# Performance work log

Hardware: AMD Instinct MI355X
Metric: run time of the kernel (lower is better)

## Reference

```python
import jax, jax.numpy as jnp
import numpy as np

B, N, DIM = 4, 1024, 768
HEADS, DIM_HEAD = 12, 64
INNER = HEADS * DIM_HEAD  # 768
SCALE = DIM ** -0.5


def setup_inputs() -> dict:
    key = jax.random.key(0)
    ks = jax.random.split(key, 5)
    return {
        "x": jax.random.normal(ks[0], (B, N, DIM), dtype=jnp.float32),
        "pos_embedding": jax.random.normal(ks[1], (B, N, DIM), dtype=jnp.float32),
        "w_qkv": jax.random.normal(ks[2], (DIM, 3 * INNER), dtype=jnp.float32) * (DIM ** -0.5),
        "w_qk_pos": jax.random.normal(ks[3], (DIM, 2 * INNER), dtype=jnp.float32) * (DIM ** -0.5),
        "w_out": jax.random.normal(ks[4], (INNER, DIM), dtype=jnp.float32) * (INNER ** -0.5),
        "b_out": jnp.zeros((DIM,), dtype=jnp.float32),
    }


def _split_heads(t):
    # [b, n, h*d] -> [b, h, n, d]
    b, n, _ = t.shape
    return t.reshape(b, n, HEADS, DIM_HEAD).transpose(0, 2, 1, 3)


def reference(x, pos_embedding, w_qkv, w_qk_pos, w_out, b_out):
    qkv = x @ w_qkv  # [b, n, 3*inner]
    q, k, v = (_split_heads(t) for t in jnp.split(qkv, 3, axis=-1))
    qk_pos = pos_embedding @ w_qk_pos  # [b, n, 2*inner]
    q_pos, k_pos = (_split_heads(t) for t in jnp.split(qk_pos, 2, axis=-1))

    dots = jnp.einsum('bhid,bhjd->bhij', q, k) * SCALE
    dots_pos = jnp.einsum('bhid,bhjd->bhij', q_pos, k_pos) * SCALE
    dots = (dots + dots_pos) * 0.5  # averaged content+positional scores

    attn = jax.nn.softmax(dots, axis=-1)
    out = jnp.einsum('bhij,bhjd->bhid', attn, v)
    out = out.transpose(0, 2, 1, 3).reshape(x.shape[0], x.shape[1], INNER)
    return out @ w_out + b_out
```

## Files before the change

kernel.cpp:

```cpp
#include <hip/hip_runtime.h>
#include <cstdint>
#include <cstddef>

typedef __bf16 bf16;
typedef __bf16 bf16x8 __attribute__((ext_vector_type(8)));
typedef __bf16 bf16x4v __attribute__((ext_vector_type(4)));
typedef float  f32x4  __attribute__((ext_vector_type(4)));

#define MFMA(a, b, c) __builtin_amdgcn_mfma_f32_16x16x32_bf16((a), (b), (c), 0, 0, 0)

typedef __attribute__((address_space(3))) unsigned int  lds_u32;
typedef __attribute__((address_space(1))) unsigned int glob_u32;


__global__ void k_cvt2(const float* __restrict__ x, const float* __restrict__ pos,
                       bf16* __restrict__ xb, bf16* __restrict__ posb) {
    int i = blockIdx.x * 256 + threadIdx.x;
    const float* in = x; bf16* out = xb;
    if (i >= 786432) { i -= 786432; in = pos; out = posb; }
    float4 v = reinterpret_cast<const float4*>(in)[i];
    bf16x4v o; o[0] = (bf16)v.x; o[1] = (bf16)v.y; o[2] = (bf16)v.z; o[3] = (bf16)v.w;
    reinterpret_cast<bf16x4v*>(out)[i] = o;
}

__global__ void k_tr(const float* __restrict__ w_qkv, const float* __restrict__ w_qk_pos,
                     const float* __restrict__ w_out,
                     bf16* __restrict__ wqkvT, bf16* __restrict__ wqkposT,
                     bf16* __restrict__ woutT) {
    __shared__ float t[32][33];
    int bx = blockIdx.x;
    const float* in; bf16* out; int N;
    if (bx < 72)       { in = w_qkv;    out = wqkvT;   N = 2304; }
    else if (bx < 120) { in = w_qk_pos; out = wqkposT; N = 1536; bx -= 72; }
    else               { in = w_out;    out = woutT;   N = 768;  bx -= 120; }
    const int n0 = bx * 32, k0 = blockIdx.y * 32;
    const int tx = threadIdx.x & 31, ty = threadIdx.x >> 5;
#pragma unroll
    for (int r = 0; r < 32; r += 8)
        t[ty + r][tx] = in[(size_t)(k0 + ty + r) * N + n0 + tx];
    __syncthreads();
#pragma unroll
    for (int r = 0; r < 32; r += 8)
        out[(size_t)(n0 + ty + r) * 768 + k0 + tx] = (bf16)t[tx][ty + r];
}

__launch_bounds__(256, 3)
__global__ void k_gemm12(const bf16* __restrict__ xb, const bf16* __restrict__ posb,
                         const bf16* __restrict__ wqkvT, const bf16* __restrict__ wqkposT,
                         bf16* __restrict__ qcat, bf16* __restrict__ kcat,
                         bf16* __restrict__ vT) {
    __shared__ bf16 lA[2][128][32];
    __shared__ bf16 lB[2][128][32];

    const int tid  = threadIdx.x;
    const int lane = tid & 63, wave = tid >> 6;
    const int quad = lane >> 4, col = lane & 15;
    const int sw2  = (col >> 1) & 3;
    const int wm = (wave >> 1) * 64, wn = (wave & 1) * 64;

    const int fid = blockIdx.x;
    const int xcd = fid & 7, s = fid >> 3;
    const int sx = s % 15, sy = s / 15;
    int bx = (xcd & 1) * 15 + sx;
    const int by = (xcd >> 1) * 8 + sy;

    int mode, nBase;
    const bf16 *A, *BT;
    if (bx < 18) { mode = 0; A = xb;   BT = wqkvT;   nBase = bx * 128; }
    else         { mode = 1; A = posb; BT = wqkposT; nBase = (bx - 18) * 128; }
    const int mBase = by * 128;

    const bf16* Ap = A  + (size_t)mBase * 768;
    const bf16* Bp = BT + (size_t)nBase * 768;

#define STAGE12(buf, k0)                                                        \
    _Pragma("unroll")                                                           \
    for (int j = 0; j < 2; ++j) {                                               \
        int idx = (wave * 2 + j) * 64 + lane;                                   \
        int row = idx >> 2, c = (idx & 3) ^ ((row >> 1) & 3);                   \
        __builtin_amdgcn_global_load_lds(                                       \
            (const glob_u32*)(Ap + (size_t)row * 768 + (k0) + c * 8),           \
            (lds_u32*)((char*)&lA[buf][0][0] + (wave * 2 + j) * 1024), 16, 0, 0);\
        __builtin_amdgcn_global_load_lds(                                       \
            (const glob_u32*)(Bp + (size_t)row * 768 + (k0) + c * 8),           \
            (lds_u32*)((char*)&lB[buf][0][0] + (wave * 2 + j) * 1024), 16, 0, 0);\
    }

    f32x4 acc[4][4];
#pragma unroll
    for (int mi = 0; mi < 4; ++mi)
#pragma unroll
        for (int ni = 0; ni < 4; ++ni) acc[mi][ni] = f32x4{0.f, 0.f, 0.f, 0.f};

    STAGE12(0, 0)
    for (int it = 0; it < 24; ++it) {
        const int cur = it & 1, nxt = cur ^ 1;
        __syncthreads();
        if (it < 23) STAGE12(nxt, (it + 1) * 32)

        bf16x8 af[4], bfg[4];
#pragma unroll
        for (int mi = 0; mi < 4; ++mi)
            af[mi]  = *(const bf16x8*)&lA[cur][wm + mi * 16 + col][(quad ^ sw2) * 8];
#pragma unroll
        for (int ni = 0; ni < 4; ++ni)
            bfg[ni] = *(const bf16x8*)&lB[cur][wn + ni * 16 + col][(quad ^ sw2) * 8];
#pragma unroll
        for (int mi = 0; mi < 4; ++mi)
#pragma unroll
            for (int ni = 0; ni < 4; ++ni)
                acc[mi][ni] = MFMA(af[mi], bfg[ni], acc[mi][ni]);
    }
#undef STAGE12

    const int bb = mBase >> 10;
    const int sr0 = (mBase & 1023) + wm + quad * 4;
#pragma unroll
    for (int ni = 0; ni < 4; ++ni) {
        const int nb = nBase + wn + ni * 16;
        const int which = (mode == 0) ? (nb >= 1536 ? 2 : (nb >= 768 ? 1 : 0))
                                      : (nb >= 768 ? 1 : 0);
        const int rem = nb - which * 768;
        const int hh = rem >> 6, dd0 = rem & 63;
        const size_t hb = (size_t)(bb * 12 + hh);
        if (mode == 0 && which == 2) {
            bf16* dstv = vT + (hb * 64 + dd0 + col) * 1024 + sr0;
#pragma unroll
            for (int mi = 0; mi < 4; ++mi) {
                bf16x4v pk;
#pragma unroll
                for (int r = 0; r < 4; ++r) pk[r] = (bf16)acc[mi][ni][r];
                *(bf16x4v*)(dstv + mi * 16) = pk;
            }
        } else {
            bf16* dstq = (which == 0 ? qcat : kcat)
                       + (hb * 1024 + sr0) * 128 + (mode == 1 ? 64 : 0) + dd0 + col;
#pragma unroll
            for (int mi = 0; mi < 4; ++mi)
#pragma unroll
                for (int r = 0; r < 4; ++r)
                    dstq[(size_t)(mi * 16 + r) * 128] = (bf16)acc[mi][ni][r];
        }
    }
}

__launch_bounds__(256, 3)
__global__ void k_attn(const bf16* __restrict__ qcat, const bf16* __restrict__ kcat,
                       const bf16* __restrict__ vT, bf16* __restrict__ attn_out) {
    __shared__ bf16 lK[2][64][128];
    __shared__ bf16 lV[2][64][64];
    __shared__ bf16 lP[4][16][40];

    const int tid  = threadIdx.x;
    const int lane = tid & 63, wave = tid >> 6;
    const int quad = lane >> 4, col = lane & 15;
    const int sw   = col & 7;

    const int fid = blockIdx.x;
    const int xcd = fid & 7, s = fid >> 3;
    const int qt = s & 15;
    const int unit = (s >> 4) * 8 + xcd;
    const int b = unit / 12, h = unit % 12;

    const size_t hrow = (size_t)(b * 12 + h) * 1024;
    const bf16* Kb = kcat + hrow * 128;
    const bf16* Vb = vT + (size_t)(b * 12 + h) * 64 * 1024;

    const int kidx = wave * 256 + lane;
    const int vidx = wave * 128 + lane;

#define STAGE_K(buf, kv0)                                                      \
    _Pragma("unroll")                                                          \
    for (int j = 0; j < 4; ++j) {                                              \
        int idx = kidx + j * 64;                                               \
        int row = idx >> 4, c = idx & 15, csrc = c ^ (row & 7);                \
        __builtin_amdgcn_global_load_lds(                                      \
            (const glob_u32*)(Kb + (size_t)((kv0) + row) * 128 + csrc * 8),    \
            (lds_u32*)(&lK[buf][0][0] + (wave * 4 + j) * 512), 16, 0, 0);      \
    }
#define STAGE_V(buf, kv0)                                                      \
    _Pragma("unroll")                                                          \
    for (int j = 0; j < 2; ++j) {                                              \
        int idx = vidx + j * 64;                                               \
        int row = idx >> 3, c = idx & 7, csrc = c ^ (row & 7);                 \
        __builtin_amdgcn_global_load_lds(                                      \
            (const glob_u32*)(Vb + (size_t)row * 1024 + (kv0) + csrc * 8),     \
            (lds_u32*)(&lV[buf][0][0] + (wave * 2 + j) * 512), 16, 0, 0);      \
    }

    bf16x8 qf[4];
    {
        const bf16* qrow = qcat + (hrow + qt * 64 + wave * 16 + col) * 128;
#pragma unroll
        for (int f = 0; f < 4; ++f) qf[f] = *(const bf16x8*)(qrow + f * 32 + quad * 8);
    }

    f32x4 o[4];
#pragma unroll
    for (int t = 0; t < 4; ++t) o[t] = f32x4{0.f, 0.f, 0.f, 0.f};
    float lsum[4] = {0.f, 0.f, 0.f, 0.f};
    const float c2 = 0.018042195912f * 1.44269504089f;

    STAGE_K(0, 0)
    STAGE_V(0, 0)

    for (int it = 0; it < 16; ++it) {
        const int cur = it & 1, nxt = cur ^ 1;
        __syncthreads();
        if (it < 15) {
            const int kv1 = (it + 1) * 64;
            STAGE_K(nxt, kv1)
            STAGE_V(nxt, kv1)
        }

        f32x4 s4[4];
#pragma unroll
        for (int t = 0; t < 4; ++t) s4[t] = f32x4{0.f, 0.f, 0.f, 0.f};
#pragma unroll
        for (int t = 0; t < 4; ++t)
#pragma unroll
            for (int f = 0; f < 4; ++f) {
                bf16x8 kf = *(const bf16x8*)&lK[cur][t * 16 + col][((f * 4 + quad) ^ sw) * 8];
                s4[t] = MFMA(qf[f], kf, s4[t]);
            }

#pragma unroll
        for (int t = 0; t < 4; ++t)
#pragma unroll
            for (int r = 0; r < 4; ++r) s4[t][r] = exp2f(s4[t][r] * c2);
#pragma unroll
        for (int r = 0; r < 4; ++r)
            lsum[r] += (s4[0][r] + s4[1][r]) + (s4[2][r] + s4[3][r]);

#pragma unroll
        for (int half = 0; half < 2; ++half) {
#pragma unroll
            for (int r = 0; r < 4; ++r)
#pragma unroll
                for (int t2 = 0; t2 < 2; ++t2)
                    lP[wave][quad * 4 + r][t2 * 16 + col] = (bf16)s4[half * 2 + t2][r];
            bf16x8 pf = *(const bf16x8*)&lP[wave][col][quad * 8];
#pragma unroll
            for (int t = 0; t < 4; ++t) {
                bf16x8 vf = *(const bf16x8*)&lV[cur][t * 16 + col][((half * 4 + quad) ^ sw) * 8];
                o[t] = MFMA(pf, vf, o[t]);
            }
        }
    }

#pragma unroll
    for (int r = 0; r < 4; ++r) {
        float l = lsum[r];
#pragma unroll
        for (int off = 1; off < 16; off <<= 1) l += __shfl_xor(l, off, 64);
        float inv = 1.f / l;
        int row = qt * 64 + wave * 16 + quad * 4 + r;
#pragma unroll
        for (int t = 0; t < 4; ++t)
            attn_out[((size_t)b * 1024 + row) * 768 + h * 64 + t * 16 + col] =
                (bf16)(o[t][r] * inv);
    }
#undef STAGE_K
#undef STAGE_V
}

__launch_bounds__(256, 3)
__global__ void k_gemm_out(const bf16* __restrict__ aout, const bf16* __restrict__ woutT,
                           const float* __restrict__ bias, float* __restrict__ out) {
    __shared__ bf16 lA[2][128][32];
    __shared__ bf16 lB[2][64][32];

    const int tid  = threadIdx.x;
    const int lane = tid & 63, wave = tid >> 6;
    const int quad = lane >> 4, col = lane & 15;
    const int sw2  = (col >> 1) & 3;
    const int wm = (wave >> 1) * 64, wn = (wave & 1) * 32;

    const int fid = blockIdx.x;
    const int xcd = fid & 7, s = fid >> 3;
    const int sx = s % 6, sy = s / 6;
    const int bx = (xcd & 1) * 6 + sx;
    const int by = (xcd >> 1) * 8 + sy;

    const int mBase = by * 128, nBase = bx * 64;

    const bf16* Ap = aout  + (size_t)mBase * 768;
    const bf16* Bp = woutT + (size_t)nBase * 768;

#define STAGE_O(buf, k0)                                                        \
    _Pragma("unroll")                                                           \
    for (int j = 0; j < 2; ++j) {                                               \
        int idx = (wave * 2 + j) * 64 + lane;                                   \
        int row = idx >> 2, c = (idx & 3) ^ ((row >> 1) & 3);                   \
        __builtin_amdgcn_global_load_lds(                                       \
            (const glob_u32*)(Ap + (size_t)row * 768 + (k0) + c * 8),           \
            (lds_u32*)((char*)&lA[buf][0][0] + (wave * 2 + j) * 1024), 16, 0, 0);\
    }                                                                           \
    {                                                                           \
        int idx = wave * 64 + lane;                                             \
        int row = idx >> 2, c = (idx & 3) ^ ((row >> 1) & 3);                   \
        __builtin_amdgcn_global_load_lds(                                       \
            (const glob_u32*)(Bp + (size_t)row * 768 + (k0) + c * 8),           \
            (lds_u32*)((char*)&lB[buf][0][0] + wave * 1024), 16, 0, 0);         \
    }

    f32x4 acc[4][2];
#pragma unroll
    for (int mi = 0; mi < 4; ++mi)
#pragma unroll
        for (int ni = 0; ni < 2; ++ni) acc[mi][ni] = f32x4{0.f, 0.f, 0.f, 0.f};

    STAGE_O(0, 0)
    for (int it = 0; it < 24; ++it) {
        const int cur = it & 1, nxt = cur ^ 1;
        __syncthreads();
        if (it < 23) STAGE_O(nxt, (it + 1) * 32)

        bf16x8 af[4], bfg[2];
#pragma unroll
        for (int mi = 0; mi < 4; ++mi)
            af[mi]  = *(const bf16x8*)&lA[cur][wm + mi * 16 + col][(quad ^ sw2) * 8];
#pragma unroll
        for (int ni = 0; ni < 2; ++ni)
            bfg[ni] = *(const bf16x8*)&lB[cur][wn + ni * 16 + col][(quad ^ sw2) * 8];
#pragma unroll
        for (int mi = 0; mi < 4; ++mi)
#pragma unroll
            for (int ni = 0; ni < 2; ++ni)
                acc[mi][ni] = MFMA(af[mi], bfg[ni], acc[mi][ni]);
    }
#undef STAGE_O

#pragma unroll
    for (int mi = 0; mi < 4; ++mi)
#pragma unroll
        for (int ni = 0; ni < 2; ++ni)
#pragma unroll
            for (int r = 0; r < 4; ++r) {
                int m = mBase + wm + mi * 16 + quad * 4 + r;
                int n = nBase + wn + ni * 16 + col;
                out[(size_t)m * 768 + n] = acc[mi][ni][r] + bias[n];
            }
}

extern "C" void kernel_launch(void* const* d_in, const int* in_sizes, int n_in,
                              void* d_out, int out_size, void* d_ws, size_t ws_size,
                              hipStream_t stream) {
    const float* x        = (const float*)d_in[0];
    const float* pos      = (const float*)d_in[1];
    const float* w_qkv    = (const float*)d_in[2];
    const float* w_qk_pos = (const float*)d_in[3];
    const float* w_out    = (const float*)d_in[4];
    const float* b_out    = (const float*)d_in[5];
    float* out = (float*)d_out;

    char* ws = (char*)d_ws;
    bf16* xb      = (bf16*)(ws);
    bf16* posb    = (bf16*)(ws + 6291456);
    bf16* wqkvT   = (bf16*)(ws + 12582912);
    bf16* wqkposT = (bf16*)(ws + 16121856);
    bf16* woutT   = (bf16*)(ws + 18481152);
    bf16* qcat    = (bf16*)(ws + 19660800);
    bf16* kcat    = (bf16*)(ws + 32243712);
    bf16* vT      = (bf16*)(ws + 44826624);
    bf16* aout    = (bf16*)(ws + 51118080);

    k_cvt2<<<6144, 256, 0, stream>>>(x, pos, xb, posb);
    k_tr<<<dim3(144, 24), 256, 0, stream>>>(w_qkv, w_qk_pos, w_out, wqkvT, wqkposT, woutT);
    k_gemm12<<<960, 256, 0, stream>>>(xb, posb, wqkvT, wqkposT, qcat, kcat, vT);
    k_attn<<<768, 256, 0, stream>>>(qcat, kcat, vT, aout);
    k_gemm_out<<<384, 256, 0, stream>>>(aout, woutT, b_out, out);
}
```

Measured before the change: 191.6 us.

## Split attention KV range across waves with register operands and LDS reduction

The attention kernel now has each wave own a slice of the key/value sequence for all 64 queries, instead of each wave owning 16 query rows and sweeping every key. K and V fragments are read straight from global memory into registers, so LDS staging and per-iteration barriers are gone. The softmax probabilities stay in registers as MFMA operands by computing S transposed (K·Q), which removes the LDS round-trip for P. Partial outputs and row sums are combined across waves through a float LDS reduction at the end. The softmax scale is folded into Q at the projection GEMM, and occupancy is lowered to 2 blocks per SM because of larger register and LDS use; uncoalesced global K/V loads add risk.

```diff
diff --git a/kernel.cpp b/kernel.cpp
--- a/kernel.cpp
+++ b/kernel.cpp
@@ -113,6 +113,7 @@
     }
 #undef STAGE12
 
+    const float c2s = 0.018042195912f * 1.44269504089f;
     const int bb = mBase >> 10;
     const int sr0 = (mBase & 1023) + wm + quad * 4;
 #pragma unroll
@@ -133,28 +134,28 @@
                 *(bf16x4v*)(dstv + mi * 16) = pk;
             }
         } else {
+            const float scl = (which == 0) ? c2s : 1.0f;
             bf16* dstq = (which == 0 ? qcat : kcat)
                        + (hb * 1024 + sr0) * 128 + (mode == 1 ? 64 : 0) + dd0 + col;
 #pragma unroll
             for (int mi = 0; mi < 4; ++mi)
 #pragma unroll
                 for (int r = 0; r < 4; ++r)
-                    dstq[(size_t)(mi * 16 + r) * 128] = (bf16)acc[mi][ni][r];
-        }
-    }
-}
-
-__launch_bounds__(256, 3)
+                    dstq[(size_t)(mi * 16 + r) * 128] = (bf16)(acc[mi][ni][r] * scl);
+        }
+    }
+}
+
+__launch_bounds__(256, 2)
 __global__ void k_attn(const bf16* __restrict__ qcat, const bf16* __restrict__ kcat,
                        const bf16* __restrict__ vT, bf16* __restrict__ attn_out) {
-    __shared__ bf16 lK[2][64][128];
-    __shared__ bf16 lV[2][64][64];
-    __shared__ bf16 lP[4][16][40];
+    __shared__ float lRed[4][64][68];
+    __shared__ float lS[16][64];
+    __shared__ float lSinv[64];
 
     const int tid  = threadIdx.x;
     const int lane = tid & 63, wave = tid >> 6;
     const int quad = lane >> 4, col = lane & 15;
-    const int sw   = col & 7;
 
     const int fid = blockIdx.x;
     const int xcd = fid & 7, s = fid >> 3;
@@ -162,106 +163,109 @@
     const int unit = (s >> 4) * 8 + xcd;
     const int b = unit / 12, h = unit % 12;
 
-    const size_t hrow = (size_t)(b * 12 + h) * 1024;
-    const bf16* Kb = kcat + hrow * 128;
-    const bf16* Vb = vT + (size_t)(b * 12 + h) * 64 * 1024;
-
-    const int kidx = wave * 256 + lane;
-    const int vidx = wave * 128 + lane;
-
-#define STAGE_K(buf, kv0)                                                      \
-    _Pragma("unroll")                                                          \
-    for (int j = 0; j < 4; ++j) {                                              \
-        int idx = kidx + j * 64;                                               \
-        int row = idx >> 4, c = idx & 15, csrc = c ^ (row & 7);                \
-        __builtin_amdgcn_global_load_lds(                                      \
-            (const glob_u32*)(Kb + (size_t)((kv0) + row) * 128 + csrc * 8),    \
-            (lds_u32*)(&lK[buf][0][0] + (wave * 4 + j) * 512), 16, 0, 0);      \
-    }
-#define STAGE_V(buf, kv0)                                                      \
-    _Pragma("unroll")                                                          \
-    for (int j = 0; j < 2; ++j) {                                              \
-        int idx = vidx + j * 64;                                               \
-        int row = idx >> 3, c = idx & 7, csrc = c ^ (row & 7);                 \
-        __builtin_amdgcn_global_load_lds(                                      \
-            (const glob_u32*)(Vb + (size_t)row * 1024 + (kv0) + csrc * 8),     \
-            (lds_u32*)(&lV[buf][0][0] + (wave * 2 + j) * 512), 16, 0, 0);      \
-    }
-
-    bf16x8 qf[4];
-    {
-        const bf16* qrow = qcat + (hrow + qt * 64 + wave * 16 + col) * 128;
-#pragma unroll
-        for (int f = 0; f < 4; ++f) qf[f] = *(const bf16x8*)(qrow + f * 32 + quad * 8);
-    }
-
-    f32x4 o[4];
-#pragma unroll
-    for (int t = 0; t < 4; ++t) o[t] = f32x4{0.f, 0.f, 0.f, 0.f};
-    float lsum[4] = {0.f, 0.f, 0.f, 0.f};
-    const float c2 = 0.018042195912f * 1.44269504089f;
-
-    STAGE_K(0, 0)
-    STAGE_V(0, 0)
-
-    for (int it = 0; it < 16; ++it) {
-        const int cur = it & 1, nxt = cur ^ 1;
-        __syncthreads();
-        if (it < 15) {
-            const int kv1 = (it + 1) * 64;
-            STAGE_K(nxt, kv1)
-            STAGE_V(nxt, kv1)
-        }
-
-        f32x4 s4[4];
-#pragma unroll
-        for (int t = 0; t < 4; ++t) s4[t] = f32x4{0.f, 0.f, 0.f, 0.f};
-#pragma unroll
-        for (int t = 0; t < 4; ++t)
-#pragma unroll
-            for (int f = 0; f < 4; ++f) {
-                bf16x8 kf = *(const bf16x8*)&lK[cur][t * 16 + col][((f * 4 + quad) ^ sw) * 8];
-                s4[t] = MFMA(qf[f], kf, s4[t]);
-            }
-
-#pragma unroll
-        for (int t = 0; t < 4; ++t)
-#pragma unroll
-            for (int r = 0; r < 4; ++r) s4[t][r] = exp2f(s4[t][r] * c2);
-#pragma unroll
-        for (int r = 0; r < 4; ++r)
-            lsum[r] += (s4[0][r] + s4[1][r]) + (s4[2][r] + s4[3][r]);
-
-#pragma unroll
-        for (int half = 0; half < 2; ++half) {
-#pragma unroll
-            for (int r = 0; r < 4; ++r)
-#pragma unroll
-                for (int t2 = 0; t2 < 2; ++t2)
-                    lP[wave][quad * 4 + r][t2 * 16 + col] = (bf16)s4[half * 2 + t2][r];
-            bf16x8 pf = *(const bf16x8*)&lP[wave][col][quad * 8];
-#pragma unroll
-            for (int t = 0; t < 4; ++t) {
-                bf16x8 vf = *(const bf16x8*)&lV[cur][t * 16 + col][((half * 4 + quad) ^ sw) * 8];
-                o[t] = MFMA(pf, vf, o[t]);
-            }
-        }
-    }
-
-#pragma unroll
-    for (int r = 0; r < 4; ++r) {
-        float l = lsum[r];
-#pragma unroll
-        for (int off = 1; off < 16; off <<= 1) l += __shfl_xor(l, off, 64);
-        float inv = 1.f / l;
-        int row = qt * 64 + wave * 16 + quad * 4 + r;
-#pragma unroll
-        for (int t = 0; t < 4; ++t)
-            attn_out[((size_t)b * 1024 + row) * 768 + h * 64 + t * 16 + col] =
-                (bf16)(o[t][r] * inv);
-    }
-#undef STAGE_K
-#undef STAGE_V
+    const bf16* Qb = qcat + (size_t)unit * 1024 * 128;
+    const bf16* Kb = kcat + (size_t)unit * 1024 * 128;
+    const bf16* Vb = vT   + (size_t)unit * 64 * 1024;
+
+    bf16x8 qb[4][4];
+#pragma unroll
+    for (int nt = 0; nt < 4; ++nt) {
+        const bf16* qrow = Qb + (size_t)(qt * 64 + nt * 16 + col) * 128;
+#pragma unroll
+        for (int f = 0; f < 4; ++f)
+            qb[nt][f] = *(const bf16x8*)(qrow + f * 32 + quad * 8);
+    }
+
+    f32x4 o[4][4];
+#pragma unroll
+    for (int vt = 0; vt < 4; ++vt)
+#pragma unroll
+        for (int nt = 0; nt < 4; ++nt) o[vt][nt] = f32x4{0.f, 0.f, 0.f, 0.f};
+    float ps[4] = {0.f, 0.f, 0.f, 0.f};
+
+    const int kvw = wave * 16;
+
+    for (int itp = 0; itp < 8; ++itp) {
+        const int kvA = itp * 128 + kvw;
+        const int kvB = kvA + 64;
+
+        bf16x8 kfA[4], kfB[4];
+#pragma unroll
+        for (int f = 0; f < 4; ++f) {
+            kfA[f] = *(const bf16x8*)(Kb + (size_t)(kvA + col) * 128 + f * 32 + quad * 8);
+            kfB[f] = *(const bf16x8*)(Kb + (size_t)(kvB + col) * 128 + f * 32 + quad * 8);
+        }
+        bf16x8 vf[4];
+#pragma unroll
+        for (int vt = 0; vt < 4; ++vt) {
+            bf16x4v va = *(const bf16x4v*)(Vb + (size_t)(vt * 16 + col) * 1024 + kvA + quad * 4);
+            bf16x4v vb = *(const bf16x4v*)(Vb + (size_t)(vt * 16 + col) * 1024 + kvB + quad * 4);
+#pragma unroll
+            for (int i = 0; i < 4; ++i) { vf[vt][i] = va[i]; vf[vt][4 + i] = vb[i]; }
+        }
+
+        bf16x8 pbf[4];
+#pragma unroll
+        for (int nt = 0; nt < 4; ++nt) {
+            f32x4 st = f32x4{0.f, 0.f, 0.f, 0.f};
+#pragma unroll
+            for (int f = 0; f < 4; ++f) st = MFMA(kfA[f], qb[nt][f], st);
+            float p0 = exp2f(st[0]), p1 = exp2f(st[1]);
+            float p2 = exp2f(st[2]), p3 = exp2f(st[3]);
+            ps[nt] += (p0 + p1) + (p2 + p3);
+            pbf[nt][0] = (bf16)p0; pbf[nt][1] = (bf16)p1;
+            pbf[nt][2] = (bf16)p2; pbf[nt][3] = (bf16)p3;
+        }
+#pragma unroll
+        for (int nt = 0; nt < 4; ++nt) {
+            f32x4 st = f32x4{0.f, 0.f, 0.f, 0.f};
+#pragma unroll
+            for (int f = 0; f < 4; ++f) st = MFMA(kfB[f], qb[nt][f], st);
+            float p0 = exp2f(st[0]), p1 = exp2f(st[1]);
+            float p2 = exp2f(st[2]), p3 = exp2f(st[3]);
+            ps[nt] += (p0 + p1) + (p2 + p3);
+            pbf[nt][4] = (bf16)p0; pbf[nt][5] = (bf16)p1;
+            pbf[nt][6] = (bf16)p2; pbf[nt][7] = (bf16)p3;
+        }
+#pragma unroll
+        for (int vt = 0; vt < 4; ++vt)
+#pragma unroll
+            for (int nt = 0; nt < 4; ++nt)
+                o[vt][nt] = MFMA(vf[vt], pbf[nt], o[vt][nt]);
+    }
+
+#pragma unroll
+    for (int vt = 0; vt < 4; ++vt)
+#pragma unroll
+        for (int nt = 0; nt < 4; ++nt)
+            *(f32x4*)&lRed[wave][nt * 16 + col][vt * 16 + quad * 4] = o[vt][nt];
+#pragma unroll
+    for (int nt = 0; nt < 4; ++nt)
+        lS[wave * 4 + quad][nt * 16 + col] = ps[nt];
+    __syncthreads();
+
+    if (tid < 64) {
+        float t = 0.f;
+#pragma unroll
+        for (int w = 0; w < 16; ++w) t += lS[w][tid];
+        lSinv[tid] = 1.f / t;
+    }
+    __syncthreads();
+
+#pragma unroll
+    for (int cix = 0; cix < 4; ++cix) {
+        int c = cix * 256 + tid;
+        int q = c >> 4, v4 = (c & 15) * 4;
+        f32x4 acc = *(const f32x4*)&lRed[0][q][v4];
+        acc += *(const f32x4*)&lRed[1][q][v4];
+        acc += *(const f32x4*)&lRed[2][q][v4];
+        acc += *(const f32x4*)&lRed[3][q][v4];
+        float inv = lSinv[q];
+        bf16x4v pk;
+#pragma unroll
+        for (int i = 0; i < 4; ++i) pk[i] = (bf16)(acc[i] * inv);
+        *(bf16x4v*)(attn_out + ((size_t)b * 1024 + qt * 64 + q) * 768 + h * 64 + v4) = pk;
+    }
 }
 
 __launch_bounds__(256, 3)
```

After: 196.8 us. 2.7% more time.

## Transpose attention scores to drop LDS P round-trip; load GEMM B operand directly

Applied to the files above, without the earlier changes.

The attention kernel now computes S^T (K as the A operand, Q as B), so each lane holds a query column of probabilities. These can be packed straight into the B operand of the PV MFMA, which removes the per-wave LDS staging of P and the extra barrier-free LDS traffic. The softmax scale is folded into the q-part of qcat in the projection GEMM epilogue, and the row-sum reduction is reduced to two shuffles. The QKV GEMM also drops LDS staging for the weight operand, using register double-buffered global loads instead. That trades LDS traffic for uncoalesced-ish global loads, and changes the output store pattern to contiguous per-row writes.

```diff
diff --git a/kernel.cpp b/kernel.cpp
--- a/kernel.cpp
+++ b/kernel.cpp
@@ -50,7 +50,6 @@
                          bf16* __restrict__ qcat, bf16* __restrict__ kcat,
                          bf16* __restrict__ vT) {
     __shared__ bf16 lA[2][128][32];
-    __shared__ bf16 lB[2][128][32];
 
     const int tid  = threadIdx.x;
     const int lane = tid & 63, wave = tid >> 6;
@@ -73,7 +72,7 @@
     const bf16* Ap = A  + (size_t)mBase * 768;
     const bf16* Bp = BT + (size_t)nBase * 768;
 
-#define STAGE12(buf, k0)                                                        \
+#define STAGE_A(buf, k0)                                                        \
     _Pragma("unroll")                                                           \
     for (int j = 0; j < 2; ++j) {                                               \
         int idx = (wave * 2 + j) * 64 + lane;                                   \
@@ -81,10 +80,16 @@
         __builtin_amdgcn_global_load_lds(                                       \
             (const glob_u32*)(Ap + (size_t)row * 768 + (k0) + c * 8),           \
             (lds_u32*)((char*)&lA[buf][0][0] + (wave * 2 + j) * 1024), 16, 0, 0);\
-        __builtin_amdgcn_global_load_lds(                                       \
-            (const glob_u32*)(Bp + (size_t)row * 768 + (k0) + c * 8),           \
-            (lds_u32*)((char*)&lB[buf][0][0] + (wave * 2 + j) * 1024), 16, 0, 0);\
-    }
+    }
+
+    const bf16* Bq[4];
+#pragma unroll
+    for (int ni = 0; ni < 4; ++ni)
+        Bq[ni] = Bp + (size_t)(wn + ni * 16 + col) * 768 + quad * 8;
+
+    bf16x8 bcur[4], bnxt[4];
+#pragma unroll
+    for (int ni = 0; ni < 4; ++ni) bcur[ni] = *(const bf16x8*)(Bq[ni]);
 
     f32x4 acc[4][4];
 #pragma unroll
@@ -92,27 +97,32 @@
 #pragma unroll
         for (int ni = 0; ni < 4; ++ni) acc[mi][ni] = f32x4{0.f, 0.f, 0.f, 0.f};
 
-    STAGE12(0, 0)
+    STAGE_A(0, 0)
+#pragma unroll
     for (int it = 0; it < 24; ++it) {
         const int cur = it & 1, nxt = cur ^ 1;
         __syncthreads();
-        if (it < 23) STAGE12(nxt, (it + 1) * 32)
-
-        bf16x8 af[4], bfg[4];
+        if (it < 23) {
+            STAGE_A(nxt, (it + 1) * 32)
+#pragma unroll
+            for (int ni = 0; ni < 4; ++ni)
+                bnxt[ni] = *(const bf16x8*)(Bq[ni] + (it + 1) * 32);
+        }
+        bf16x8 af[4];
 #pragma unroll
         for (int mi = 0; mi < 4; ++mi)
-            af[mi]  = *(const bf16x8*)&lA[cur][wm + mi * 16 + col][(quad ^ sw2) * 8];
-#pragma unroll
-        for (int ni = 0; ni < 4; ++ni)
-            bfg[ni] = *(const bf16x8*)&lB[cur][wn + ni * 16 + col][(quad ^ sw2) * 8];
+            af[mi] = *(const bf16x8*)&lA[cur][wm + mi * 16 + col][(quad ^ sw2) * 8];
 #pragma unroll
         for (int mi = 0; mi < 4; ++mi)
 #pragma unroll
             for (int ni = 0; ni < 4; ++ni)
-                acc[mi][ni] = MFMA(af[mi], bfg[ni], acc[mi][ni]);
-    }
-#undef STAGE12
-
+                acc[mi][ni] = MFMA(af[mi], bcur[ni], acc[mi][ni]);
+#pragma unroll
+        for (int ni = 0; ni < 4; ++ni) bcur[ni] = bnxt[ni];
+    }
+#undef STAGE_A
+
+    const float c2s = 0.018042195912f * 1.44269504089f;
     const int bb = mBase >> 10;
     const int sr0 = (mBase & 1023) + wm + quad * 4;
 #pragma unroll
@@ -133,13 +143,14 @@
                 *(bf16x4v*)(dstv + mi * 16) = pk;
             }
         } else {
+            const float scl = (which == 0) ? c2s : 1.0f;
             bf16* dstq = (which == 0 ? qcat : kcat)
                        + (hb * 1024 + sr0) * 128 + (mode == 1 ? 64 : 0) + dd0 + col;
 #pragma unroll
             for (int mi = 0; mi < 4; ++mi)
 #pragma unroll
                 for (int r = 0; r < 4; ++r)
-                    dstq[(size_t)(mi * 16 + r) * 128] = (bf16)acc[mi][ni][r];
+                    dstq[(size_t)(mi * 16 + r) * 128] = (bf16)(acc[mi][ni][r] * scl);
         }
     }
 }
@@ -149,12 +160,12 @@
                        const bf16* __restrict__ vT, bf16* __restrict__ attn_out) {
     __shared__ bf16 lK[2][64][128];
     __shared__ bf16 lV[2][64][64];
-    __shared__ bf16 lP[4][16][40];
 
     const int tid  = threadIdx.x;
     const int lane = tid & 63, wave = tid >> 6;
     const int quad = lane >> 4, col = lane & 15;
     const int sw   = col & 7;
+    const int q01  = quad >> 1, qlo = quad & 1;
 
     const int fid = blockIdx.x;
     const int xcd = fid & 7, s = fid >> 3;
@@ -162,9 +173,9 @@
     const int unit = (s >> 4) * 8 + xcd;
     const int b = unit / 12, h = unit % 12;
 
-    const size_t hrow = (size_t)(b * 12 + h) * 1024;
-    const bf16* Kb = kcat + hrow * 128;
-    const bf16* Vb = vT + (size_t)(b * 12 + h) * 64 * 1024;
+    const bf16* Qb = qcat + (size_t)unit * 1024 * 128;
+    const bf16* Kb = kcat + (size_t)unit * 1024 * 128;
+    const bf16* Vb = vT   + (size_t)unit * 64 * 1024;
 
     const int kidx = wave * 256 + lane;
     const int vidx = wave * 128 + lane;
@@ -188,18 +199,17 @@
             (lds_u32*)(&lV[buf][0][0] + (wave * 2 + j) * 512), 16, 0, 0);      \
     }
 
-    bf16x8 qf[4];
+    bf16x8 qb[4];
     {
-        const bf16* qrow = qcat + (hrow + qt * 64 + wave * 16 + col) * 128;
-#pragma unroll
-        for (int f = 0; f < 4; ++f) qf[f] = *(const bf16x8*)(qrow + f * 32 + quad * 8);
+        const bf16* qrow = Qb + (size_t)(qt * 64 + wave * 16 + col) * 128;
+#pragma unroll
+        for (int f = 0; f < 4; ++f) qb[f] = *(const bf16x8*)(qrow + f * 32 + quad * 8);
     }
 
     f32x4 o[4];
 #pragma unroll
-    for (int t = 0; t < 4; ++t) o[t] = f32x4{0.f, 0.f, 0.f, 0.f};
-    float lsum[4] = {0.f, 0.f, 0.f, 0.f};
-    const float c2 = 0.018042195912f * 1.44269504089f;
+    for (int vt = 0; vt < 4; ++vt) o[vt] = f32x4{0.f, 0.f, 0.f, 0.f};
+    float lsum = 0.f;
 
     STAGE_K(0, 0)
     STAGE_V(0, 0)
@@ -213,53 +223,56 @@
             STAGE_V(nxt, kv1)
         }
 
-        f32x4 s4[4];
-#pragma unroll
-        for (int t = 0; t < 4; ++t) s4[t] = f32x4{0.f, 0.f, 0.f, 0.f};
+        f32x4 st[4];
+#pragma unroll
+        for (int t = 0; t < 4; ++t) st[t] = f32x4{0.f, 0.f, 0.f, 0.f};
 #pragma unroll
         for (int t = 0; t < 4; ++t)
 #pragma unroll
             for (int f = 0; f < 4; ++f) {
                 bf16x8 kf = *(const bf16x8*)&lK[cur][t * 16 + col][((f * 4 + quad) ^ sw) * 8];
-                s4[t] = MFMA(qf[f], kf, s4[t]);
-            }
-
-#pragma unroll
-        for (int t = 0; t < 4; ++t)
-#pragma unroll
-            for (int r = 0; r < 4; ++r) s4[t][r] = exp2f(s4[t][r] * c2);
+                st[t] = MFMA(kf, qb[f], st[t]);
+            }
+
+        bf16x8 pbf[2];
+#pragma unroll
+        for (int c = 0; c < 2; ++c) {
+#pragma unroll
+            for (int r = 0; r < 4; ++r) {
+                float p0 = exp2f(st[2 * c][r]);
+                float p1 = exp2f(st[2 * c + 1][r]);
+                lsum += p0 + p1;
+                pbf[c][r]     = (bf16)p0;
+                pbf[c][4 + r] = (bf16)p1;
+            }
+        }
+
+#pragma unroll
+        for (int c = 0; c < 2; ++c)
+#pragma unroll
+            for (int vt = 0; vt < 4; ++vt) {
+                const bf16* vrow = &lV[cur][vt * 16 + col][0];
+                bf16x4v va = *(const bf16x4v*)(vrow + ((c * 4 + q01) ^ sw) * 8 + qlo * 4);
+                bf16x4v vb = *(const bf16x4v*)(vrow + ((c * 4 + 2 + q01) ^ sw) * 8 + qlo * 4);
+                bf16x8 vf;
+#pragma unroll
+                for (int i = 0; i < 4; ++i) { vf[i] = va[i]; vf[4 + i] = vb[i]; }
+                o[vt] = MFMA(vf, pbf[c], o[vt]);
+            }
+    }
+
+    float l = lsum;
+    l += __shfl_xor(l, 16, 64);
+    l += __shfl_xor(l, 32, 64);
+    const float inv = 1.f / l;
+
+    const int qrow = qt * 64 + wave * 16 + col;
+    bf16* dst = attn_out + ((size_t)b * 1024 + qrow) * 768 + h * 64;
+#pragma unroll
+    for (int vt = 0; vt < 4; ++vt)
 #pragma unroll
         for (int r = 0; r < 4; ++r)
-            lsum[r] += (s4[0][r] + s4[1][r]) + (s4[2][r] + s4[3][r]);
-
-#pragma unroll
-        for (int half = 0; half < 2; ++half) {
-#pragma unroll
-            for (int r = 0; r < 4; ++r)
-#pragma unroll
-                for (int t2 = 0; t2 < 2; ++t2)
-                    lP[wave][quad * 4 + r][t2 * 16 + col] = (bf16)s4[half * 2 + t2][r];
-            bf16x8 pf = *(const bf16x8*)&lP[wave][col][quad * 8];
-#pragma unroll
-            for (int t = 0; t < 4; ++t) {
-                bf16x8 vf = *(const bf16x8*)&lV[cur][t * 16 + col][((half * 4 + quad) ^ sw) * 8];
-                o[t] = MFMA(pf, vf, o[t]);
-            }
-        }
-    }
-
-#pragma unroll
-    for (int r = 0; r < 4; ++r) {
-        float l = lsum[r];
-#pragma unroll
-        for (int off = 1; off < 16; off <<= 1) l += __shfl_xor(l, off, 64);
-        float inv = 1.f / l;
-        int row = qt * 64 + wave * 16 + quad * 4 + r;
-#pragma unroll
-        for (int t = 0; t < 4; ++t)
-            attn_out[((size_t)b * 1024 + row) * 768 + h * 64 + t * 16 + col] =
-                (bf16)(o[t][r] * inv);
-    }
+            dst[vt * 16 + quad * 4 + r] = (bf16)(o[vt][r] * inv);
 #undef STAGE_K
 #undef STAGE_V
 }
```

Measured after the change: 201.5 us. +5.1%, slower.
